# Kernel optimization log

Measured on AMD Instinct MI355X. Metric: run time of the kernel, lower is better.

Reference implementation:

```python
import jax, jax.numpy as jnp
import numpy as np

HD = 256          # hidden_dim[0]
KF = 2            # k factor
KD = HD * KF      # 512, bilinear feature dim
L = 2000          # hard-coded sequence length
B = 4
NEG = np.float32(np.finfo(np.float32).min)  # finite min, NOT -inf (matches torch code)
EPS = 1e-5


def _fc(x, V, g, b):
    # weight_norm(Linear, dim=None): W = g * V / ||V||_F, then ReLU
    W = (g / jnp.linalg.norm(V)) * V  # [KD, HD]
    return jax.nn.relu(jnp.einsum('blh,kh->blk', x, W) + b)


def setup_inputs() -> dict:
    key = jax.random.key(0)
    ks = jax.random.split(key, 12)
    X = jax.random.normal(ks[0], (B, L, HD), dtype=jnp.float32)
    Y = jax.random.normal(ks[1], (B, L, HD), dtype=jnp.float32)
    mask1 = jax.random.bernoulli(ks[2], 0.8, (B, L)).astype(jnp.float32)
    mask2 = jax.random.bernoulli(ks[3], 0.8, (B, L)).astype(jnp.float32)
    # Q_net / K_net params (single weight-normed linear each)
    Qv = jax.random.normal(ks[4], (KD, HD), dtype=jnp.float32) * 0.05
    Qg = jnp.asarray(1.0, dtype=jnp.float32)
    Qb = jax.random.normal(ks[5], (KD,), dtype=jnp.float32) * 0.05
    Kv = jax.random.normal(ks[6], (KD, HD), dtype=jnp.float32) * 0.05
    Kg = jnp.asarray(1.0, dtype=jnp.float32)
    Kb = jax.random.normal(ks[7], (KD,), dtype=jnp.float32) * 0.05
    h_mat = jax.random.normal(ks[8], (KD,), dtype=jnp.float32)   # (1,1,KD) squeezed
    h_bias = jax.random.normal(ks[9], (), dtype=jnp.float32)     # (1,1,1) squeezed
    gamma = jnp.ones((KD,), dtype=jnp.float32)                   # BatchNorm1d affine
    beta = jnp.zeros((KD,), dtype=jnp.float32)
    return {"X": X, "Y": Y, "mask1": mask1, "mask2": mask2,
            "Qv": Qv, "Qg": Qg, "Qb": Qb, "Kv": Kv, "Kg": Kg, "Kb": Kb,
            "h_mat": h_mat, "h_bias": h_bias, "gamma": gamma, "beta": beta}


def _masked_softmax(A, m_row):
    # m_row: [B,1,L], broadcasts over axis 1; softmax over dim 1 as in torch
    logits = jnp.where(m_row > 0, A, NEG)
    att = jax.nn.softmax(logits, axis=1)
    return m_row * att


def reference(X, Y, mask1, mask2, Qv, Qg, Qb, Kv, Kg, Kb, h_mat, h_bias, gamma, beta):
    A1_X = _fc(X, Qv, Qg, Qb)  # [B,L,KD]
    A1_Y = _fc(Y, Kv, Kg, Kb)
    A2_Y = _fc(Y, Qv, Qg, Qb)
    A2_X = _fc(X, Kv, Kg, Kb)
    # bilinear co-attention maps [B,L,L]
    A1 = jnp.einsum('bvk,bqk->bvq', A1_X * h_mat, A1_Y) + h_bias
    A2 = jnp.einsum('bqk,bvk->bqv', A2_Y * h_mat, A2_X) + h_bias
    m1r = mask1[:, None, :]  # mask1_attend[b,v,q] = mask1[b,q]
    m2r = mask2[:, None, :]
    alpha = _masked_softmax(A1, m2r)
    logits_X = jnp.einsum('bvq,bqk->bvk', alpha, A1_Y) * mask1[:, :, None]
    beta_att = _masked_softmax(A2, m1r)
    logits_Y = jnp.einsum('bqv,bvk->bqk', beta_att, A2_X) * mask2[:, :, None]
    # AvgPool2d((2000,1)) == mean over sequence dim
    pooled = logits_X.mean(axis=1) + logits_Y.mean(axis=1)  # [B,KD]
    # BatchNorm1d training-mode forward (biased batch stats)
    mu = pooled.mean(axis=0)
    var = pooled.var(axis=0)
    return gamma * (pooled - mu) * jax.lax.rsqrt(var + EPS) + beta
```

## Files before the change

### kernel.cpp

```cpp
#include <hip/hip_runtime.h>

#define NB 4
#define LSEQ 2000
#define HD 256
#define KD 512
#define LPAD 2048
#define SMALL_N 18562

using short8 = __attribute__((ext_vector_type(8))) short;
using f32x4  = __attribute__((ext_vector_type(4))) float;
typedef unsigned short u16;

__device__ __forceinline__ float b2f(u16 u) { return __uint_as_float(((unsigned)u) << 16); }
__device__ __forceinline__ u16 f2b(float f) {
    unsigned u = __float_as_uint(f);
    u += 0x7FFFu + ((u >> 16) & 1u);
    return (u16)(u >> 16);
}
__device__ __forceinline__ bool detect32(const void* gamma) {
    return ((const float*)gamma)[0] == 1.0f;
}
__device__ __forceinline__ void gl_lds16(const u16* g, short* l) {
    __builtin_amdgcn_global_load_lds(
        (const __attribute__((address_space(1))) unsigned int*)g,
        (__attribute__((address_space(3))) unsigned int*)l, 16, 0, 0);
}

__global__ void convert_kernel(const void* X, const void* Y, const void* Qv, const void* Kv,
                               const void* m1, const void* m2, const void* Qb, const void* Kb,
                               const void* hm, const void* Qg, const void* Kg,
                               const void* gamma, const void* beta,
                               u16* __restrict__ Xb, u16* __restrict__ Yb,
                               u16* __restrict__ Qvb, u16* __restrict__ Kvb,
                               float* __restrict__ smallf, float* __restrict__ ssq)
{
    const bool is32 = detect32(gamma);
    const int seg = blockIdx.y;
    if (seg < 4) {
        const void* src = seg == 0 ? X : seg == 1 ? Y : seg == 2 ? Qv : Kv;
        u16* dst = seg == 0 ? Xb : seg == 1 ? Yb : seg == 2 ? Qvb : Kvb;
        const int n = (seg < 2) ? NB * LSEQ * HD : KD * HD;
        const int i0 = (blockIdx.x * 256 + threadIdx.x) * 8;
        if (i0 >= n) return;
        uint4 pack;
        u16* v = (u16*)&pack;
        if (is32) {
            float4 fa = ((const float4*)src)[(i0 >> 2)];
            float4 fb = ((const float4*)src)[(i0 >> 2) + 1];
            v[0] = f2b(fa.x); v[1] = f2b(fa.y); v[2] = f2b(fa.z); v[3] = f2b(fa.w);
            v[4] = f2b(fb.x); v[5] = f2b(fb.y); v[6] = f2b(fb.z); v[7] = f2b(fb.w);
        } else {
            pack = ((const uint4*)src)[i0 >> 3];
        }
        ((uint4*)dst)[i0 >> 3] = pack;
        if (seg >= 2) {
            float s = 0.f;
            #pragma unroll
            for (int j = 0; j < 8; ++j) { float f = b2f(v[j]); s = fmaf(f, f, s); }
            #pragma unroll
            for (int off = 32; off > 0; off >>= 1) s += __shfl_xor(s, off);
            if ((threadIdx.x & 63) == 0) atomicAdd(&ssq[seg - 2], s);
        }
    } else {
        const int i0 = (blockIdx.x * 256 + threadIdx.x) * 4;
        for (int i = i0; i < i0 + 4; ++i) {
            if (i >= SMALL_N) break;
            const void* src; int off;
            if      (i <  8000) { src = m1;    off = i; }
            else if (i < 16000) { src = m2;    off = i - 8000; }
            else if (i < 16512) { src = Qb;    off = i - 16000; }
            else if (i < 17024) { src = Kb;    off = i - 16512; }
            else if (i < 17536) { src = hm;    off = i - 17024; }
            else if (i < 18048) { src = gamma; off = i - 17536; }
            else if (i < 18560) { src = beta;  off = i - 18048; }
            else if (i == 18560) {
                float f = ((const float*)Qg)[0];
                smallf[i] = (f == 1.0f) ? 1.0f : b2f(((const u16*)Qg)[0]);
                continue;
            } else {
                float f = ((const float*)Kg)[0];
                smallf[i] = (f == 1.0f) ? 1.0f : b2f(((const u16*)Kg)[0]);
                continue;
            }
            smallf[i] = is32 ? ((const float*)src)[off] : b2f(((const u16*)src)[off]);
        }
    }
}

__global__ __launch_bounds__(256, 2)
void fc_kernel(const u16* __restrict__ X, const u16* __restrict__ Y,
               const u16* __restrict__ Qv, const u16* __restrict__ Kv,
               const float* __restrict__ Qbf, const float* __restrict__ Kbf,
               const float* __restrict__ hf, const float* __restrict__ gv,
               const float* __restrict__ ssq, u16* __restrict__ fc)
{
    const int mt = blockIdx.x, nt = blockIdx.y, t = blockIdx.z;
    const int b = t >> 2, which = t & 3;
    const u16* In = ((which == 0) | (which == 3)) ? (X + (size_t)b * LSEQ * HD)
                                                  : (Y + (size_t)b * LSEQ * HD);
    const bool isQ = (which == 0) | (which == 2);
    const u16* W      = isQ ? Qv : Kv;
    const float* bias = isQ ? Qbf : Kbf;
    const int j = isQ ? 0 : 1;
    const float s = gv[j] / sqrtf(ssq[j]);
    u16* out = fc + (size_t)t * LSEQ * KD;

    __shared__ __align__(16) short As[2][128 * 32];
    __shared__ __align__(16) short Bs[2][128 * 32];

    const int tid = threadIdx.x;
    const int lane = tid & 63, wave = tid >> 6;
    const int wm = wave >> 1, wn = wave & 1;
    const int quad = lane >> 4, l15 = lane & 15;
    const int sr = tid >> 2, sc = tid & 3;
    const int scz = sc ^ ((sr >> 1) & 3);
    const int m0 = mt * 128, n0 = nt * 128;

    int gm0 = min(m0 + sr, LSEQ - 1), gm1 = min(m0 + sr + 64, LSEQ - 1);
    const u16* pA0 = In + (size_t)gm0 * HD + scz * 8;
    const u16* pA1 = In + (size_t)gm1 * HD + scz * 8;
    const u16* pB0 = W + (size_t)(n0 + sr) * HD + scz * 8;
    const u16* pB1 = W + (size_t)(n0 + sr + 64) * HD + scz * 8;
    const int dof = sr * 32 + sc * 8;

    int aoff[4], boff[4];
    #pragma unroll
    for (int i = 0; i < 4; ++i) {
        int ra = wm * 64 + i * 16 + l15;
        aoff[i] = ra * 32 + (quad ^ ((ra >> 1) & 3)) * 8;
        int rb = wn * 64 + i * 16 + l15;
        boff[i] = rb * 32 + (quad ^ ((rb >> 1) & 3)) * 8;
    }

    gl_lds16(pA0, &As[0][dof]);
    gl_lds16(pA1, &As[0][64 * 32 + dof]);
    gl_lds16(pB0, &Bs[0][dof]);
    gl_lds16(pB1, &Bs[0][64 * 32 + dof]);
    __syncthreads();

    f32x4 acc[4][4] = {};

    for (int kt = 0; kt < 8; ++kt) {
        const int cur = kt & 1, nxt = cur ^ 1;
        if (kt < 7) {
            const int ko = (kt + 1) * 32;
            gl_lds16(pA0 + ko, &As[nxt][dof]);
            gl_lds16(pA1 + ko, &As[nxt][64 * 32 + dof]);
            gl_lds16(pB0 + ko, &Bs[nxt][dof]);
            gl_lds16(pB1 + ko, &Bs[nxt][64 * 32 + dof]);
        }
        short8 af[4], bf[4];
        #pragma unroll
        for (int i = 0; i < 4; ++i) af[i] = *(const short8*)&As[cur][aoff[i]];
        #pragma unroll
        for (int i = 0; i < 4; ++i) bf[i] = *(const short8*)&Bs[cur][boff[i]];
        #pragma unroll
        for (int mi = 0; mi < 4; ++mi)
            #pragma unroll
            for (int ni = 0; ni < 4; ++ni)
                acc[mi][ni] = __builtin_amdgcn_mfma_f32_16x16x32_bf16(af[mi], bf[ni], acc[mi][ni], 0, 0, 0);
        __syncthreads();
    }

    #pragma unroll
    for (int ni = 0; ni < 4; ++ni) {
        int n = n0 + wn * 64 + ni * 16 + l15;
        float bv = bias[n];
        float hv = isQ ? hf[n] : 1.0f;
        #pragma unroll
        for (int mi = 0; mi < 4; ++mi) {
            int mb = m0 + wm * 64 + mi * 16 + quad * 4;
            #pragma unroll
            for (int r = 0; r < 4; ++r) {
                int m = mb + r;
                if (m < LSEQ) {
                    float v = fmaf(s, acc[mi][ni][r], bv);
                    v = v > 0.f ? v : 0.f;
                    out[(size_t)m * KD + n] = f2b(v * hv);
                }
            }
        }
    }
}

__global__ __launch_bounds__(512, 2)
void colsm_kernel(const u16* __restrict__ fc, const float* __restrict__ m1f,
                  const float* __restrict__ m2f,
                  float* __restrict__ part_d, float* __restrict__ part_n)
{
    const int vs = blockIdx.x, qt = blockIdx.y, z = blockIdx.z;
    const int a = z >> 2, b = z & 3;
    const u16* R  = fc + (size_t)(b * 4 + (a == 0 ? 1 : 3)) * LSEQ * KD;
    const u16* Sm = fc + (size_t)(b * 4 + (a == 0 ? 0 : 2)) * LSEQ * KD;
    const float* wmask = (a == 0 ? m1f : m2f) + (size_t)b * LSEQ;

    __shared__ __align__(16) short AL[4][256 * 32];
    __shared__ __align__(16) short BL[4][256 * 32];

    const int tid = threadIdx.x;
    const int lane = tid & 63, wave = tid >> 6;
    const int wm = wave >> 2, wn = wave & 3;
    const int quad = lane >> 4, l15 = lane & 15;
    const int r0 = qt * 256, c0 = vs * 256;

    const int srow = tid >> 2;
    const int kslot = (tid & 3) ^ ((tid >> 3) & 3);
    int grA0 = min(r0 + srow, LSEQ - 1), grA1 = min(r0 + 128 + srow, LSEQ - 1);
    int gcB0 = min(c0 + srow, LSEQ - 1), gcB1 = min(c0 + 128 + srow, LSEQ - 1);
    const u16* pRa = R  + (size_t)grA0 * KD + kslot * 8;
    const u16* pRb = R  + (size_t)grA1 * KD + kslot * 8;
    const u16* pSa = Sm + (size_t)gcB0 * KD + kslot * 8;
    const u16* pSb = Sm + (size_t)gcB1 * KD + kslot * 8;
    const int ldst = tid * 8;

    const int swz = (quad ^ ((l15 >> 1) & 3)) * 8;

    #define STAGE_A(h) { short* d_ = &AL[(h) & 3][ldst];               \
                         gl_lds16(pRa + (h) * 32, d_);                 \
                         gl_lds16(pRb + (h) * 32, d_ + 4096); }
    #define STAGE_B(h) { short* d_ = &BL[(h) & 3][ldst];               \
                         gl_lds16(pSa + (h) * 32, d_);                 \
                         gl_lds16(pSb + (h) * 32, d_ + 4096); }

    STAGE_A(0); STAGE_B(0); STAGE_A(1); STAGE_B(1); STAGE_A(2); STAGE_B(2);
    asm volatile("s_waitcnt vmcnt(4)" ::: "memory");
    __builtin_amdgcn_s_barrier();
    __builtin_amdgcn_sched_barrier(0);

    f32x4 acc[8][4] = {};
    short8 bf[4];

    #pragma unroll 2
    for (int t = 0; t < 8; ++t) {
        #pragma unroll
        for (int p = 0; p < 4; ++p) {
            const int j = 2 * t + (p >> 1);
            const short* Ab = AL[j & 3];
            const short* Bb = BL[j & 3];
            short8 af[4];
            #pragma unroll
            for (int mi = 0; mi < 4; ++mi) {
                int lr = wm * 128 + (p & 1) * 64 + mi * 16 + l15;
                af[mi] = *(const short8*)&Ab[lr * 32 + swz];
            }
            if ((p & 1) == 0) {
                #pragma unroll
                for (int ni = 0; ni < 4; ++ni) {
                    int lc = wn * 64 + ni * 16 + l15;
                    bf[ni] = *(const short8*)&Bb[lc * 32 + swz];
                }
            }
            if (p == 0)      { if (2 * t + 3 <= 15) STAGE_A(2 * t + 3); }
            else if (p == 1) { if (2 * t + 3 <= 15) STAGE_B(2 * t + 3); }
            else if (p == 2) { if (2 * t + 4 <= 15) STAGE_A(2 * t + 4); }
            else {
                if (2 * t + 4 <= 15) STAGE_B(2 * t + 4);
                if (t < 6)       asm volatile("s_waitcnt vmcnt(4)" ::: "memory");
                else if (t == 6) asm volatile("s_waitcnt vmcnt(0)" ::: "memory");
            }
            asm volatile("" ::: "memory");
            __builtin_amdgcn_s_barrier();
            __builtin_amdgcn_sched_barrier(0);
            __builtin_amdgcn_s_setprio(1);
            #pragma unroll
            for (int mi = 0; mi < 4; ++mi)
                #pragma unroll
                for (int ni = 0; ni < 4; ++ni)
                    acc[(p & 1) * 4 + mi][ni] =
                        __builtin_amdgcn_mfma_f32_16x16x32_bf16(af[mi], bf[ni],
                                                                acc[(p & 1) * 4 + mi][ni], 0, 0, 0);
            __builtin_amdgcn_s_setprio(0);
            asm volatile("" ::: "memory");
            __builtin_amdgcn_s_barrier();
            __builtin_amdgcn_sched_barrier(0);
        }
    }

    __syncthreads();
    float* ldsD = (float*)&AL[0][0];
    float* ldsN = (float*)&AL[1][0];

    float wv[4], vv[4];
    #pragma unroll
    for (int ni = 0; ni < 4; ++ni) {
        int cg = c0 + wn * 64 + ni * 16 + l15;
        bool valid = cg < LSEQ;
        vv[ni] = valid ? 1.f : 0.f;
        wv[ni] = valid ? wmask[min(cg, LSEQ - 1)] : 0.f;
    }
    #pragma unroll
    for (int aq = 0; aq < 8; ++aq)
        #pragma unroll
        for (int r = 0; r < 4; ++r) {
            float d = 0.f, n = 0.f;
            #pragma unroll
            for (int ni = 0; ni < 4; ++ni) {
                float e = __expf(acc[aq][ni][r]);
                d = fmaf(vv[ni], e, d);
                n = fmaf(wv[ni], e, n);
            }
            #pragma unroll
            for (int off = 1; off < 16; off <<= 1) {
                d += __shfl_xor(d, off);
                n += __shfl_xor(n, off);
            }
            if (l15 == 0) {
                int row = wm * 128 + (aq >> 2) * 64 + (aq & 3) * 16 + quad * 4 + r;
                ldsD[row * 4 + wn] = d;
                ldsN[row * 4 + wn] = n;
            }
        }
    __syncthreads();
    if (tid < 256) {
        int q = r0 + tid;
        if (q < LSEQ) {
            size_t p = ((size_t)(z * 8 + vs)) * LPAD + q;
            part_d[p] = ldsD[tid * 4 + 0] + ldsD[tid * 4 + 1] + ldsD[tid * 4 + 2] + ldsD[tid * 4 + 3];
            part_n[p] = ldsN[tid * 4 + 0] + ldsN[tid * 4 + 1] + ldsN[tid * 4 + 2] + ldsN[tid * 4 + 3];
        }
    }
    #undef STAGE_A
    #undef STAGE_B
}

__global__ void combine_kernel(const float* __restrict__ part_d, const float* __restrict__ part_n,
                               const float* __restrict__ m1f, const float* __restrict__ m2f,
                               float* __restrict__ c, float* __restrict__ pooled)
{
    int idx = blockIdx.x * 256 + threadIdx.x;
    if (idx < NB * KD) pooled[idx] = 0.f;
    int z = idx >> 11, q = idx & (LPAD - 1);
    int a = z >> 2, b = z & 3;
    float d = 0.f, n = 0.f;
    #pragma unroll
    for (int vs = 0; vs < 8; ++vs) {
        size_t p = ((size_t)(z * 8 + vs)) * LPAD + q;
        d += part_d[p]; n += part_n[p];
    }
    float val = 0.f;
    if (q < LSEQ) {
        float om = (a == 0 ? m2f : m1f)[b * LSEQ + q];
        val = om * n / d;
    }
    c[(size_t)z * LPAD + q] = val;
}

__global__ void pooled_kernel(const u16* __restrict__ fc, const float* __restrict__ c,
                              float* __restrict__ pooled)
{
    const int b = blockIdx.x, rs = blockIdx.y;
    const int k = threadIdx.x;
    const u16* YK = fc + (size_t)(b * 4 + 1) * LSEQ * KD;
    const u16* XK = fc + (size_t)(b * 4 + 3) * LSEQ * KD;
    const float* c1 = c + (size_t)(0 + b) * LPAD;
    const float* c2 = c + (size_t)(4 + b) * LPAD;
    float s = 0.f;
    const int rbeg = rs * 50, rend = rbeg + 50;
    for (int r = rbeg; r < rend; ++r) {
        s = fmaf(c1[r], b2f(YK[(size_t)r * KD + k]), s);
        s = fmaf(c2[r], b2f(XK[(size_t)r * KD + k]), s);
    }
    atomicAdd(&pooled[b * KD + k], s * (1.0f / LSEQ));
}

__global__ void ln_kernel(const float* __restrict__ pooled, const float* __restrict__ gammaf,
                          const float* __restrict__ betaf, const void* __restrict__ gamma_orig,
                          void* __restrict__ out)
{
    int k = blockIdx.x * 256 + threadIdx.x;
    float p[NB];
    #pragma unroll
    for (int b = 0; b < NB; ++b) p[b] = pooled[b * KD + k];
    float mu = 0.25f * (p[0] + p[1] + p[2] + p[3]);
    float var = 0.f;
    #pragma unroll
    for (int b = 0; b < NB; ++b) { float d = p[b] - mu; var = fmaf(d, d, var); }
    var *= 0.25f;
    float inv = rsqrtf(var + 1e-5f);
    float g = gammaf[k], be = betaf[k];
    const bool is32 = detect32(gamma_orig);
    #pragma unroll
    for (int b = 0; b < NB; ++b) {
        float v = fmaf(g * (p[b] - mu), inv, be);
        if (is32) ((float*)out)[b * KD + k] = v;
        else      ((u16*)out)[b * KD + k] = f2b(v);
    }
}

extern "C" void kernel_launch(void* const* d_in, const int* in_sizes, int n_in,
                              void* d_out, int out_size, void* d_ws, size_t ws_size,
                              hipStream_t stream)
{
    const void* X  = d_in[0];
    const void* Y  = d_in[1];
    const void* m1 = d_in[2];
    const void* m2 = d_in[3];
    const void* Qv = d_in[4];
    const void* Qg = d_in[5];
    const void* Qb = d_in[6];
    const void* Kv = d_in[7];
    const void* Kg = d_in[8];
    const void* Kb = d_in[9];
    const void* h  = d_in[10];
    const void* gamma = d_in[12];
    const void* beta  = d_in[13];

    char* ws = (char*)d_ws;
    size_t off = 0;
    u16* Xb  = (u16*)(ws + off); off += (size_t)NB * LSEQ * HD * 2;
    u16* Yb  = (u16*)(ws + off); off += (size_t)NB * LSEQ * HD * 2;
    u16* Qvb = (u16*)(ws + off); off += (size_t)KD * HD * 2;
    u16* Kvb = (u16*)(ws + off); off += (size_t)KD * HD * 2;
    float* smallf = (float*)(ws + off); off += ((size_t)(SMALL_N + 2) * 4 + 15) / 16 * 16;
    u16* fc  = (u16*)(ws + off); off += (size_t)16 * LSEQ * KD * 2;
    float* part_d = (float*)(ws + off); off += (size_t)8 * 8 * LPAD * 4;
    float* part_n = (float*)(ws + off); off += (size_t)8 * 8 * LPAD * 4;
    float* c      = (float*)(ws + off); off += (size_t)8 * LPAD * 4;
    float* pooled = (float*)(ws + off); off += (size_t)NB * KD * 4;

    const float* m1f = smallf;
    const float* m2f = smallf + 8000;
    const float* Qbf = smallf + 16000;
    const float* Kbf = smallf + 16512;
    const float* hf  = smallf + 17024;
    const float* gmf = smallf + 17536;
    const float* bef = smallf + 18048;
    const float* gv  = smallf + 18560;
    float* ssq = smallf + SMALL_N;

    hipMemsetAsync(ssq, 0, 2 * sizeof(float), stream);
    convert_kernel<<<dim3(1000, 5), 256, 0, stream>>>(X, Y, Qv, Kv, m1, m2, Qb, Kb, h, Qg, Kg,
                                                      gamma, beta, Xb, Yb, Qvb, Kvb, smallf, ssq);
    fc_kernel     <<<dim3(16, 4, 16), 256, 0, stream>>>(Xb, Yb, Qvb, Kvb, Qbf, Kbf, hf, gv, ssq, fc);
    colsm_kernel  <<<dim3(8, 8, 8), 512, 0, stream>>>(fc, m1f, m2f, part_d, part_n);
    combine_kernel<<<64, 256, 0, stream>>>(part_d, part_n, m1f, m2f, c, pooled);
    pooled_kernel <<<dim3(4, 40), 512, 0, stream>>>(fc, c, pooled);
    ln_kernel     <<<2, 256, 0, stream>>>(pooled, gmf, bef, gamma, d_out);
}
```

Measured before the change: 193.4 us.

## Process two column tiles per colsm block and remap blocks for XCD locality

The colsm kernel now launches 256 blocks instead of 512. Each block computes two adjacent 256-column tiles, pipelining the loads of the second tile straight after the first, and the epilogue runs after each tile. Block indices are remapped so blocks that share row tiles and batches land on the same XCD, which should improve L2 reuse. The aim is to amortize pipeline warm-up and drain and to reuse the A operand via cache. In exchange there are fewer blocks, which means less parallelism on the 256 CUs, and the epilogue's extra LDS buffers and syncs are added.

```diff
diff --git a/kernel.cpp b/kernel.cpp
--- a/kernel.cpp
+++ b/kernel.cpp
@@ -188,7 +188,11 @@
                   const float* __restrict__ m2f,
                   float* __restrict__ part_d, float* __restrict__ part_n)
 {
-    const int vs = blockIdx.x, qt = blockIdx.y, z = blockIdx.z;
+    const int n = blockIdx.x;
+    const int xcd = n & 7, rest = n >> 3;
+    const int qt = (xcd >> 2) * 4 + (rest & 3);
+    const int z  = rest >> 2;
+    const int vs0 = (xcd & 3) * 2;
     const int a = z >> 2, b = z & 3;
     const u16* R  = fc + (size_t)(b * 4 + (a == 0 ? 1 : 3)) * LSEQ * KD;
     const u16* Sm = fc + (size_t)(b * 4 + (a == 0 ? 0 : 2)) * LSEQ * KD;
@@ -196,31 +200,38 @@
 
     __shared__ __align__(16) short AL[4][256 * 32];
     __shared__ __align__(16) short BL[4][256 * 32];
+    __shared__ float ldsD[256][4];
+    __shared__ float ldsN[256][4];
 
     const int tid = threadIdx.x;
     const int lane = tid & 63, wave = tid >> 6;
     const int wm = wave >> 2, wn = wave & 3;
     const int quad = lane >> 4, l15 = lane & 15;
-    const int r0 = qt * 256, c0 = vs * 256;
+    const int r0 = qt * 256;
 
     const int srow = tid >> 2;
     const int kslot = (tid & 3) ^ ((tid >> 3) & 3);
     int grA0 = min(r0 + srow, LSEQ - 1), grA1 = min(r0 + 128 + srow, LSEQ - 1);
-    int gcB0 = min(c0 + srow, LSEQ - 1), gcB1 = min(c0 + 128 + srow, LSEQ - 1);
-    const u16* pRa = R  + (size_t)grA0 * KD + kslot * 8;
-    const u16* pRb = R  + (size_t)grA1 * KD + kslot * 8;
-    const u16* pSa = Sm + (size_t)gcB0 * KD + kslot * 8;
-    const u16* pSb = Sm + (size_t)gcB1 * KD + kslot * 8;
+    const u16* pRa = R + (size_t)grA0 * KD + kslot * 8;
+    const u16* pRb = R + (size_t)grA1 * KD + kslot * 8;
+    const int c00 = vs0 * 256, c01 = c00 + 256;
+    int g0a = min(c00 + srow, LSEQ - 1), g1a = min(c00 + 128 + srow, LSEQ - 1);
+    int g0b = min(c01 + srow, LSEQ - 1), g1b = min(c01 + 128 + srow, LSEQ - 1);
+    const u16* pSa0 = Sm + (size_t)g0a * KD + kslot * 8;
+    const u16* pSb0 = Sm + (size_t)g1a * KD + kslot * 8;
+    const u16* pSa1 = Sm + (size_t)g0b * KD + kslot * 8;
+    const u16* pSb1 = Sm + (size_t)g1b * KD + kslot * 8;
     const int ldst = tid * 8;
-
     const int swz = (quad ^ ((l15 >> 1) & 3)) * 8;
 
-    #define STAGE_A(h) { short* d_ = &AL[(h) & 3][ldst];               \
-                         gl_lds16(pRa + (h) * 32, d_);                 \
-                         gl_lds16(pRb + (h) * 32, d_ + 4096); }
-    #define STAGE_B(h) { short* d_ = &BL[(h) & 3][ldst];               \
-                         gl_lds16(pSa + (h) * 32, d_);                 \
-                         gl_lds16(pSb + (h) * 32, d_ + 4096); }
+    #define STAGE_A(H) { short* d_ = &AL[(H) & 3][ldst];                     \
+                         gl_lds16(pRa + ((H) & 15) * 32, d_);                \
+                         gl_lds16(pRb + ((H) & 15) * 32, d_ + 4096); }
+    #define STAGE_B(H) { const u16* sa_ = ((H) & 16) ? pSa1 : pSa0;          \
+                         const u16* sb_ = ((H) & 16) ? pSb1 : pSb0;          \
+                         short* d_ = &BL[(H) & 3][ldst];                     \
+                         gl_lds16(sa_ + ((H) & 15) * 32, d_);                \
+                         gl_lds16(sb_ + ((H) & 15) * 32, d_ + 4096); }
 
     STAGE_A(0); STAGE_B(0); STAGE_A(1); STAGE_B(1); STAGE_A(2); STAGE_B(2);
     asm volatile("s_waitcnt vmcnt(4)" ::: "memory");
@@ -230,8 +241,7 @@
     f32x4 acc[8][4] = {};
     short8 bf[4];
 
-    #pragma unroll 2
-    for (int t = 0; t < 8; ++t) {
+    auto ktile = [&](int t) {
         #pragma unroll
         for (int p = 0; p < 4; ++p) {
             const int j = 2 * t + (p >> 1);
@@ -250,13 +260,13 @@
                     bf[ni] = *(const short8*)&Bb[lc * 32 + swz];
                 }
             }
-            if (p == 0)      { if (2 * t + 3 <= 15) STAGE_A(2 * t + 3); }
-            else if (p == 1) { if (2 * t + 3 <= 15) STAGE_B(2 * t + 3); }
-            else if (p == 2) { if (2 * t + 4 <= 15) STAGE_A(2 * t + 4); }
+            if (p == 0)      { if (2 * t + 3 <= 31) STAGE_A(2 * t + 3); }
+            else if (p == 1) { if (2 * t + 3 <= 31) STAGE_B(2 * t + 3); }
+            else if (p == 2) { if (2 * t + 4 <= 31) STAGE_A(2 * t + 4); }
             else {
-                if (2 * t + 4 <= 15) STAGE_B(2 * t + 4);
-                if (t < 6)       asm volatile("s_waitcnt vmcnt(4)" ::: "memory");
-                else if (t == 6) asm volatile("s_waitcnt vmcnt(0)" ::: "memory");
+                if (2 * t + 4 <= 31) STAGE_B(2 * t + 4);
+                if (t < 14)       asm volatile("s_waitcnt vmcnt(4)" ::: "memory");
+                else if (t == 14) asm volatile("s_waitcnt vmcnt(0)" ::: "memory");
             }
             asm volatile("" ::: "memory");
             __builtin_amdgcn_s_barrier();
@@ -274,51 +284,62 @@
             __builtin_amdgcn_s_barrier();
             __builtin_amdgcn_sched_barrier(0);
         }
-    }
-
-    __syncthreads();
-    float* ldsD = (float*)&AL[0][0];
-    float* ldsN = (float*)&AL[1][0];
-
-    float wv[4], vv[4];
-    #pragma unroll
-    for (int ni = 0; ni < 4; ++ni) {
-        int cg = c0 + wn * 64 + ni * 16 + l15;
-        bool valid = cg < LSEQ;
-        vv[ni] = valid ? 1.f : 0.f;
-        wv[ni] = valid ? wmask[min(cg, LSEQ - 1)] : 0.f;
-    }
+    };
+
+    auto epi = [&](int c0, int vs) {
+        float wv[4], vv[4];
+        #pragma unroll
+        for (int ni = 0; ni < 4; ++ni) {
+            int cg = c0 + wn * 64 + ni * 16 + l15;
+            bool valid = cg < LSEQ;
+            vv[ni] = valid ? 1.f : 0.f;
+            wv[ni] = valid ? wmask[min(cg, LSEQ - 1)] : 0.f;
+        }
+        #pragma unroll
+        for (int aq = 0; aq < 8; ++aq)
+            #pragma unroll
+            for (int r = 0; r < 4; ++r) {
+                float d = 0.f, nn = 0.f;
+                #pragma unroll
+                for (int ni = 0; ni < 4; ++ni) {
+                    float e = __expf(acc[aq][ni][r]);
+                    d = fmaf(vv[ni], e, d);
+                    nn = fmaf(wv[ni], e, nn);
+                }
+                #pragma unroll
+                for (int off = 1; off < 16; off <<= 1) {
+                    d += __shfl_xor(d, off);
+                    nn += __shfl_xor(nn, off);
+                }
+                if (l15 == 0) {
+                    int row = wm * 128 + (aq >> 2) * 64 + (aq & 3) * 16 + quad * 4 + r;
+                    ldsD[row][wn] = d;
+                    ldsN[row][wn] = nn;
+                }
+            }
+        __syncthreads();
+        if (tid < 256) {
+            int q = r0 + tid;
+            if (q < LSEQ) {
+                size_t pp = ((size_t)(z * 8 + vs)) * LPAD + q;
+                part_d[pp] = ldsD[tid][0] + ldsD[tid][1] + ldsD[tid][2] + ldsD[tid][3];
+                part_n[pp] = ldsN[tid][0] + ldsN[tid][1] + ldsN[tid][2] + ldsN[tid][3];
+            }
+        }
+        __syncthreads();
+    };
+
+    #pragma unroll 2
+    for (int t = 0; t < 8; ++t) ktile(t);
+    epi(c00, vs0);
     #pragma unroll
     for (int aq = 0; aq < 8; ++aq)
         #pragma unroll
-        for (int r = 0; r < 4; ++r) {
-            float d = 0.f, n = 0.f;
-            #pragma unroll
-            for (int ni = 0; ni < 4; ++ni) {
-                float e = __expf(acc[aq][ni][r]);
-                d = fmaf(vv[ni], e, d);
-                n = fmaf(wv[ni], e, n);
-            }
-            #pragma unroll
-            for (int off = 1; off < 16; off <<= 1) {
-                d += __shfl_xor(d, off);
-                n += __shfl_xor(n, off);
-            }
-            if (l15 == 0) {
-                int row = wm * 128 + (aq >> 2) * 64 + (aq & 3) * 16 + quad * 4 + r;
-                ldsD[row * 4 + wn] = d;
-                ldsN[row * 4 + wn] = n;
-            }
-        }
-    __syncthreads();
-    if (tid < 256) {
-        int q = r0 + tid;
-        if (q < LSEQ) {
-            size_t p = ((size_t)(z * 8 + vs)) * LPAD + q;
-            part_d[p] = ldsD[tid * 4 + 0] + ldsD[tid * 4 + 1] + ldsD[tid * 4 + 2] + ldsD[tid * 4 + 3];
-            part_n[p] = ldsN[tid * 4 + 0] + ldsN[tid * 4 + 1] + ldsN[tid * 4 + 2] + ldsN[tid * 4 + 3];
-        }
-    }
+        for (int ni = 0; ni < 4; ++ni)
+            acc[aq][ni] = (f32x4){0.f, 0.f, 0.f, 0.f};
+    #pragma unroll 2
+    for (int t = 8; t < 16; ++t) ktile(t);
+    epi(c01, vs0 + 1);
     #undef STAGE_A
     #undef STAGE_B
 }
@@ -432,7 +453,7 @@
     convert_kernel<<<dim3(1000, 5), 256, 0, stream>>>(X, Y, Qv, Kv, m1, m2, Qb, Kb, h, Qg, Kg,
                                                       gamma, beta, Xb, Yb, Qvb, Kvb, smallf, ssq);
     fc_kernel     <<<dim3(16, 4, 16), 256, 0, stream>>>(Xb, Yb, Qvb, Kvb, Qbf, Kbf, hf, gv, ssq, fc);
-    colsm_kernel  <<<dim3(8, 8, 8), 512, 0, stream>>>(fc, m1f, m2f, part_d, part_n);
+    colsm_kernel  <<<256, 512, 0, stream>>>(fc, m1f, m2f, part_d, part_n);
     combine_kernel<<<64, 256, 0, stream>>>(part_d, part_n, m1f, m2f, c, pooled);
     pooled_kernel <<<dim3(4, 40), 512, 0, stream>>>(fc, c, pooled);
     ln_kernel     <<<2, 256, 0, stream>>>(pooled, gmf, bef, gamma, d_out);
```

Result: faster. 188.4 us (-2.6%).
